# Kernel optimization log

Measured on AMD Instinct MI355X. Metric: run time of the kernel, lower is better.

Reference implementation:

```python
import jax, jax.numpy as jnp
import numpy as np

C = 512
H = 8

def setup_inputs() -> dict:
    key = jax.random.key(0)
    ks = jax.random.split(key, 5)
    x = jax.random.normal(ks[0], (4, C, 2048), dtype=jnp.float32)
    # Conv1d(kernel_size=1) == pointwise linear: weight [out, in], bias [out]
    qkv_w = jax.random.normal(ks[1], (3 * C, C), dtype=jnp.float32) * (1.0 / np.sqrt(C))
    qkv_b = jax.random.normal(ks[2], (3 * C,), dtype=jnp.float32) * 0.02
    proj_w = jax.random.normal(ks[3], (C, C), dtype=jnp.float32) * (1.0 / np.sqrt(C))
    proj_b = jax.random.normal(ks[4], (C,), dtype=jnp.float32) * 0.02
    return {"x": x, "qkv_w": qkv_w, "qkv_b": qkv_b, "proj_w": proj_w, "proj_b": proj_b}

def reference(x, qkv_w, qkv_b, proj_w, proj_b):
    b, c, t = x.shape
    scale = c ** (-0.5)  # NOTE: full channel count, matching the torch module
    # pointwise conv: [3C, C] @ [b, C, T] -> [b, 3C, T]
    qkv = jnp.einsum('oc,bct->bot', qkv_w, x) + qkv_b[None, :, None]
    q, k, v = jnp.split(qkv, 3, axis=1)
    d = c // H
    q = q.reshape(b, H, d, t)
    k = k.reshape(b, H, d, t)
    v = v.reshape(b, H, d, t)
    attn = jnp.einsum('bhct,bhcs->bhts', q, k) * scale
    attn = jax.nn.softmax(attn, axis=-1)
    out = jnp.einsum('bhts,bhcs->bhct', attn, v)
    out = out.reshape(b, c, t)
    out = jnp.einsum('oc,bct->bot', proj_w, out) + proj_b[None, :, None]
    return x + out
```

## Files before the change

### kernel.cpp

```cpp
#include <hip/hip_runtime.h>
#include <hip/hip_bf16.h>
#include <math.h>

#define B_DIM 4
#define C_DIM 512
#define T_DIM 2048
#define H_DIM 8
#define OC3   1536
#define VN_STRIDE 2064
#define SCALE 0.044194173824159216f
#define SCALE2 (0.044194173824159216f * 1.4426950408889634f)

typedef unsigned short ushortT;
typedef unsigned int uintT;
typedef __attribute__((ext_vector_type(8))) short bf16x8;
typedef __attribute__((ext_vector_type(4))) short bf16x4;
typedef __attribute__((ext_vector_type(4))) float f32x4;

__device__ __forceinline__ ushortT f2bf(float f) {
    union { float f; uintT u; } v; v.f = f;
    uintT r = v.u + 0x7FFF + ((v.u >> 16) & 1);
    return (ushortT)(r >> 16);
}
__device__ __forceinline__ float bf2f(ushortT h) {
    union { uintT u; float f; } v; v.u = ((uintT)h) << 16;
    return v.f;
}
__device__ __forceinline__ uintT pack2bf(float a, float b) {
    uintT ua = __float_as_uint(a) + 0x8000u;
    uintT ub = __float_as_uint(b) + 0x8000u;
    return (ua >> 16) | (ub & 0xFFFF0000u);
}
__device__ __forceinline__ uintT cvtpk2bf(float a, float b) {
    union { __bf16 v[2]; uintT u; } c;
    c.v[0] = (__bf16)a; c.v[1] = (__bf16)b;
    return c.u;
}
__device__ __forceinline__ void gload_lds16(const ushortT* g, ushortT* l) {
    __builtin_amdgcn_global_load_lds(
        (const __attribute__((address_space(1))) void*)g,
        (__attribute__((address_space(3))) void*)l, 16, 0, 0);
}

__global__ __launch_bounds__(256) void prep(const float* __restrict__ x,
                                            const float* __restrict__ qw,
                                            const float* __restrict__ pw,
                                            ushortT* __restrict__ xb,
                                            ushortT* __restrict__ qwb,
                                            ushortT* __restrict__ pwb) {
    __shared__ float xs[64][65];
    const int tid = threadIdx.x;
    const int blk = blockIdx.x;
    if (blk >= 1024) {
        int idx = ((blk - 1024) * 256 + tid) * 4;
        if (idx < OC3 * C_DIM) {
            float4 v = *(const float4*)(qw + idx);
            qwb[idx + 0] = f2bf(v.x); qwb[idx + 1] = f2bf(v.y);
            qwb[idx + 2] = f2bf(v.z); qwb[idx + 3] = f2bf(v.w);
        } else {
            idx -= OC3 * C_DIM;
            float4 v = *(const float4*)(pw + idx);
            pwb[idx + 0] = f2bf(v.x); pwb[idx + 1] = f2bf(v.y);
            pwb[idx + 2] = f2bf(v.z); pwb[idx + 3] = f2bf(v.w);
        }
        return;
    }
    const int b = blk >> 8, rem = blk & 255;
    const int c0 = (rem >> 5) * 64, t0 = (rem & 31) * 64;
    #pragma unroll
    for (int it = 0; it < 4; ++it) {
        int idx = it * 256 + tid;
        int r = idx >> 4, ch = idx & 15;
        float4 v = *(const float4*)(x + ((size_t)(b * C_DIM + c0 + r)) * T_DIM + t0 + ch * 4);
        xs[r][ch * 4 + 0] = v.x; xs[r][ch * 4 + 1] = v.y;
        xs[r][ch * 4 + 2] = v.z; xs[r][ch * 4 + 3] = v.w;
    }
    __syncthreads();
    #pragma unroll
    for (int it = 0; it < 2; ++it) {
        int idx = it * 256 + tid;
        int rt = idx >> 3, ch = idx & 7;
        union { ushortT s[8]; uint4 v; } tmp;
        #pragma unroll
        for (int k = 0; k < 8; ++k) tmp.s[k] = f2bf(xs[ch * 8 + k][rt]);
        *(uint4*)(xb + ((size_t)b * T_DIM + t0 + rt) * C_DIM + c0 + ch * 8) = tmp.v;
    }
}

__global__ __launch_bounds__(256, 3) void gemm_qkv(const ushortT* __restrict__ A,
                                                   const ushortT* __restrict__ Bw,
                                                   const float* __restrict__ bias,
                                                   ushortT* __restrict__ out,
                                                   ushortT* __restrict__ Vn) {
    __shared__ __align__(16) ushortT As[8192], Bs[8192];
    const int tid = threadIdx.x, lane = tid & 63, wid = tid >> 6;
    const int u = lane & 15, q = lane >> 4;
    const int wm = wid & 1, wn = wid >> 1;
    const int m0 = blockIdx.x * 128, n0 = blockIdx.y * 128;
    const int lrow = lane >> 2, lcol = (lane & 3) * 8;

    f32x4 acc[4][4];
    const f32x4 z = {0.f, 0.f, 0.f, 0.f};
    #pragma unroll
    for (int mi = 0; mi < 4; ++mi)
        #pragma unroll
        for (int ni = 0; ni < 4; ++ni) acc[mi][ni] = z;

    for (int k0 = 0; k0 < 512; k0 += 64) {
        __syncthreads();
        gload_lds16(A  + (size_t)(m0 + wid * 32 +      lrow) * 512 + k0      + lcol, &As[(wid * 32     ) * 32]);
        gload_lds16(A  + (size_t)(m0 + wid * 32 + 16 + lrow) * 512 + k0      + lcol, &As[(wid * 32 + 16) * 32]);
        gload_lds16(A  + (size_t)(m0 + wid * 32 +      lrow) * 512 + k0 + 32 + lcol, &As[4096 + (wid * 32     ) * 32]);
        gload_lds16(A  + (size_t)(m0 + wid * 32 + 16 + lrow) * 512 + k0 + 32 + lcol, &As[4096 + (wid * 32 + 16) * 32]);
        gload_lds16(Bw + (size_t)(n0 + wid * 32 +      lrow) * 512 + k0      + lcol, &Bs[(wid * 32     ) * 32]);
        gload_lds16(Bw + (size_t)(n0 + wid * 32 + 16 + lrow) * 512 + k0      + lcol, &Bs[(wid * 32 + 16) * 32]);
        gload_lds16(Bw + (size_t)(n0 + wid * 32 +      lrow) * 512 + k0 + 32 + lcol, &Bs[4096 + (wid * 32     ) * 32]);
        gload_lds16(Bw + (size_t)(n0 + wid * 32 + 16 + lrow) * 512 + k0 + 32 + lcol, &Bs[4096 + (wid * 32 + 16) * 32]);
        __syncthreads();
        bf16x8 af[4][2], bfr[4][2];
        #pragma unroll
        for (int mi = 0; mi < 4; ++mi) {
            af[mi][0] = *(const bf16x8*)&As[(wm * 64 + mi * 16 + u) * 32 + q * 8];
            af[mi][1] = *(const bf16x8*)&As[4096 + (wm * 64 + mi * 16 + u) * 32 + q * 8];
        }
        #pragma unroll
        for (int ni = 0; ni < 4; ++ni) {
            bfr[ni][0] = *(const bf16x8*)&Bs[(wn * 64 + ni * 16 + u) * 32 + q * 8];
            bfr[ni][1] = *(const bf16x8*)&Bs[4096 + (wn * 64 + ni * 16 + u) * 32 + q * 8];
        }
        #pragma unroll
        for (int mi = 0; mi < 4; ++mi)
            #pragma unroll
            for (int ni = 0; ni < 4; ++ni) {
                acc[mi][ni] = __builtin_amdgcn_mfma_f32_16x16x32_bf16(
                    af[mi][0], bfr[ni][0], acc[mi][ni], 0, 0, 0);
                acc[mi][ni] = __builtin_amdgcn_mfma_f32_16x16x32_bf16(
                    af[mi][1], bfr[ni][1], acc[mi][ni], 0, 0, 0);
            }
    }
    if (n0 < 1024) {
        const float scl = (n0 < 512) ? SCALE2 : 1.0f;
        #pragma unroll
        for (int ni = 0; ni < 4; ++ni) {
            int o = n0 + wn * 64 + ni * 16 + u;
            float bv = bias[o];
            #pragma unroll
            for (int mi = 0; mi < 4; ++mi)
                #pragma unroll
                for (int r = 0; r < 4; ++r) {
                    int m = m0 + wm * 64 + mi * 16 + q * 4 + r;
                    out[(size_t)m * OC3 + o] = f2bf((acc[mi][ni][r] + bv) * scl);
                }
        }
    } else {
        #pragma unroll
        for (int ni = 0; ni < 4; ++ni) {
            int o = n0 + wn * 64 + ni * 16 + u;
            float bv = bias[o];
            int oo = o - 1024;
            int hv = oo >> 6, d = oo & 63;
            #pragma unroll
            for (int mi = 0; mi < 4; ++mi) {
                int m = m0 + wm * 64 + mi * 16 + q * 4;
                int b = m >> 11, t = m & 2047;
                uint2 w;
                w.x = pack2bf(acc[mi][ni][0] + bv, acc[mi][ni][1] + bv);
                w.y = pack2bf(acc[mi][ni][2] + bv, acc[mi][ni][3] + bv);
                *(uint2*)(Vn + ((size_t)((b * 8 + hv) * 64 + d)) * VN_STRIDE + t) = w;
            }
        }
    }
}

__global__ __launch_bounds__(256, 2)
void flash(const ushortT* __restrict__ qkvT, const ushortT* __restrict__ Vn,
           ushortT* __restrict__ AO)
{
    __shared__ __align__(16) ushortT smem[16384];

    const int tid = threadIdx.x, lane = tid & 63, wid = tid >> 6;
    const int u = lane & 15, q = lane >> 4;
    const int g = blockIdx.x;
    const int bh = (g & 7) * 4 + ((g >> 3) & 3);
    const int qt = g >> 5;
    const int bb = bh >> 3, h = bh & 7;
    const int q0 = qt * 128;
    const size_t qbase = (size_t)bb * T_DIM * OC3;

    bf16x8 qb[2][2];
    #pragma unroll
    for (int ti = 0; ti < 2; ++ti)
        #pragma unroll
        for (int kst = 0; kst < 2; ++kst)
            qb[ti][kst] = *(const bf16x8*)(qkvT + qbase
                + (size_t)(q0 + wid * 32 + ti * 16 + u) * OC3 + h * 64 + kst * 32 + q * 8);

    const int rs = wid * 8 + (lane >> 3);
    const int sg = (lane & 7) ^ (rs & 7);
    const ushortT* ks0 = qkvT + qbase + (size_t)(rs     ) * OC3 + 512 + h * 64 + sg * 8;
    const ushortT* ks1 = qkvT + qbase + (size_t)(rs + 32) * OC3 + 512 + h * 64 + sg * 8;
    const ushortT* vs0 = Vn + ((size_t)bh * 64 + rs     ) * VN_STRIDE + sg * 8;
    const ushortT* vs1 = Vn + ((size_t)bh * 64 + rs + 32) * VN_STRIDE + sg * 8;

    f32x4 acc[4][2];
    const f32x4 z = {0.f, 0.f, 0.f, 0.f};
    #pragma unroll
    for (int ci = 0; ci < 4; ++ci)
        #pragma unroll
        for (int ti = 0; ti < 2; ++ti) acc[ci][ti] = z;
    f32x4 lacc[2] = {z, z};
    const bf16x4 ones = {(short)0x3F80, (short)0x3F80, (short)0x3F80, (short)0x3F80};

    gload_lds16(ks0, &smem[       wid * 512]);
    gload_lds16(ks1, &smem[2048 + wid * 512]);
    gload_lds16(vs0, &smem[8192 +        wid * 512]);
    gload_lds16(vs1, &smem[8192 + 2048 + wid * 512]);
    ks0 += 64 * OC3; ks1 += 64 * OC3; vs0 += 64; vs1 += 64;
    __syncthreads();

    int cur = 0;
    for (int rnd = 0; rnd < 32; ++rnd) {
        if (rnd < 31) {
            int nb = cur ^ 1;
            gload_lds16(ks0, &smem[nb * 4096 +        wid * 512]);
            gload_lds16(ks1, &smem[nb * 4096 + 2048 + wid * 512]);
            gload_lds16(vs0, &smem[8192 + nb * 4096 +        wid * 512]);
            gload_lds16(vs1, &smem[8192 + nb * 4096 + 2048 + wid * 512]);
            ks0 += 64 * OC3; ks1 += 64 * OC3; vs0 += 64; vs1 += 64;
        }
        const ushortT* Kb = &smem[cur * 4096];
        const ushortT* Vb = &smem[8192 + cur * 4096];
        bf16x8 ka[4][2];
        #pragma unroll
        for (int si = 0; si < 4; ++si)
            #pragma unroll
            for (int kst = 0; kst < 2; ++kst)
                ka[si][kst] = *(const bf16x8*)&Kb[(si * 16 + u) * 64
                    + (((kst * 4 + q) ^ (u & 7)) * 8)];
        bf16x4 va[4][4];
        #pragma unroll
        for (int si = 0; si < 4; ++si)
            #pragma unroll
            for (int ci = 0; ci < 4; ++ci)
                va[si][ci] = *(const bf16x4*)&Vb[(ci * 16 + u) * 64
                    + (((si * 2 + (q >> 1)) ^ (u & 7)) * 8) + (q & 1) * 4];

        #pragma unroll
        for (int si = 0; si < 4; ++si) {
            f32x4 sacc[2] = {z, z};
            #pragma unroll
            for (int ti = 0; ti < 2; ++ti)
                sacc[ti] = __builtin_amdgcn_mfma_f32_16x16x32_bf16(
                    ka[si][0], qb[ti][0], sacc[ti], 0, 0, 0);
            #pragma unroll
            for (int ti = 0; ti < 2; ++ti)
                sacc[ti] = __builtin_amdgcn_mfma_f32_16x16x32_bf16(
                    ka[si][1], qb[ti][1], sacc[ti], 0, 0, 0);
            #pragma unroll
            for (int ti = 0; ti < 2; ++ti) {
                float p0 = __builtin_amdgcn_exp2f(sacc[ti][0]);
                float p1 = __builtin_amdgcn_exp2f(sacc[ti][1]);
                float p2 = __builtin_amdgcn_exp2f(sacc[ti][2]);
                float p3 = __builtin_amdgcn_exp2f(sacc[ti][3]);
                union { uint2 u2; bf16x4 v; } pw;
                pw.u2.x = cvtpk2bf(p0, p1);
                pw.u2.y = cvtpk2bf(p2, p3);
                lacc[ti] = __builtin_amdgcn_mfma_f32_16x16x16bf16_1k(
                    ones, pw.v, lacc[ti], 0, 0, 0);
                #pragma unroll
                for (int ci = 0; ci < 4; ++ci)
                    acc[ci][ti] = __builtin_amdgcn_mfma_f32_16x16x16bf16_1k(
                        va[si][ci], pw.v, acc[ci][ti], 0, 0, 0);
            }
        }
        __syncthreads();
        cur ^= 1;
    }

    ushortT* Ob = smem + wid * 2304;
    float* Lb = (float*)(smem + 9216);
    if (q == 0) {
        Lb[wid * 32 + u]      = lacc[0][0];
        Lb[wid * 32 + 16 + u] = lacc[1][0];
    }
    #pragma unroll
    for (int ci = 0; ci < 4; ++ci)
        #pragma unroll
        for (int ti = 0; ti < 2; ++ti) {
            uint2 w;
            w.x = pack2bf(acc[ci][ti][0], acc[ci][ti][1]);
            w.y = pack2bf(acc[ci][ti][2], acc[ci][ti][3]);
            *(uint2*)&Ob[(ti * 16 + u) * 72 + ci * 16 + q * 4] = w;
        }
    __syncthreads();
    {
        const int row = tid >> 1, cs = (tid & 1) * 32;
        const int w = row >> 5, r32 = row & 31;
        float linv = 1.0f / Lb[w * 32 + r32];
        const ushortT* rp = smem + w * 2304 + r32 * 72 + cs;
        size_t orow = ((size_t)bb * T_DIM + q0 + row) * C_DIM + h * 64 + cs;
        #pragma unroll
        for (int j = 0; j < 4; ++j) {
            uint4 rv = *(const uint4*)(rp + j * 8);
            const uintT* rpp = (const uintT*)&rv;
            uint4 o;
            uintT* op = (uintT*)&o;
            #pragma unroll
            for (int k = 0; k < 4; ++k)
                op[k] = pack2bf(bf2f((ushortT)(rpp[k] & 0xFFFF)) * linv,
                                bf2f((ushortT)(rpp[k] >> 16)) * linv);
            *(uint4*)(AO + orow + j * 8) = o;
        }
    }
}

__global__ __launch_bounds__(256, 2) void gemm_proj(const ushortT* __restrict__ Wp,
                                                    const ushortT* __restrict__ AOv,
                                                    const float* __restrict__ bias,
                                                    const float* __restrict__ xres,
                                                    float* __restrict__ out) {
    __shared__ __align__(16) ushortT As[8192], Bs[4096];
    const int tid = threadIdx.x, lane = tid & 63, wid = tid >> 6;
    const int u = lane & 15, q = lane >> 4;
    const int wm = wid & 1, wn = wid >> 1;
    const int m0 = blockIdx.y * 128, n0 = blockIdx.x * 64;
    const int lrow = lane >> 2, lcol = (lane & 3) * 8;

    f32x4 acc[4][2];
    const f32x4 z = {0.f, 0.f, 0.f, 0.f};
    #pragma unroll
    for (int mi = 0; mi < 4; ++mi)
        #pragma unroll
        for (int ni = 0; ni < 2; ++ni) acc[mi][ni] = z;

    for (int k0 = 0; k0 < 512; k0 += 64) {
        __syncthreads();
        gload_lds16(Wp  + (size_t)(m0 + wid * 32 +      lrow) * 512 + k0      + lcol, &As[(wid * 32     ) * 32]);
        gload_lds16(Wp  + (size_t)(m0 + wid * 32 + 16 + lrow) * 512 + k0      + lcol, &As[(wid * 32 + 16) * 32]);
        gload_lds16(Wp  + (size_t)(m0 + wid * 32 +      lrow) * 512 + k0 + 32 + lcol, &As[4096 + (wid * 32     ) * 32]);
        gload_lds16(Wp  + (size_t)(m0 + wid * 32 + 16 + lrow) * 512 + k0 + 32 + lcol, &As[4096 + (wid * 32 + 16) * 32]);
        gload_lds16(AOv + (size_t)(n0 + wid * 16 + lrow) * 512 + k0      + lcol, &Bs[(wid * 16) * 32]);
        gload_lds16(AOv + (size_t)(n0 + wid * 16 + lrow) * 512 + k0 + 32 + lcol, &Bs[2048 + (wid * 16) * 32]);
        __syncthreads();
        bf16x8 af[4][2], bfr[2][2];
        #pragma unroll
        for (int mi = 0; mi < 4; ++mi) {
            af[mi][0] = *(const bf16x8*)&As[(wm * 64 + mi * 16 + u) * 32 + q * 8];
            af[mi][1] = *(const bf16x8*)&As[4096 + (wm * 64 + mi * 16 + u) * 32 + q * 8];
        }
        #pragma unroll
        for (int ni = 0; ni < 2; ++ni) {
            bfr[ni][0] = *(const bf16x8*)&Bs[(wn * 32 + ni * 16 + u) * 32 + q * 8];
            bfr[ni][1] = *(const bf16x8*)&Bs[2048 + (wn * 32 + ni * 16 + u) * 32 + q * 8];
        }
        #pragma unroll
        for (int mi = 0; mi < 4; ++mi)
            #pragma unroll
            for (int ni = 0; ni < 2; ++ni) {
                acc[mi][ni] = __builtin_amdgcn_mfma_f32_16x16x32_bf16(
                    af[mi][0], bfr[ni][0], acc[mi][ni], 0, 0, 0);
                acc[mi][ni] = __builtin_amdgcn_mfma_f32_16x16x32_bf16(
                    af[mi][1], bfr[ni][1], acc[mi][ni], 0, 0, 0);
            }
    }
    #pragma unroll
    for (int mi = 0; mi < 4; ++mi)
        #pragma unroll
        for (int r = 0; r < 4; ++r) {
            int o = m0 + wm * 64 + mi * 16 + q * 4 + r;
            float bv = bias[o];
            #pragma unroll
            for (int ni = 0; ni < 2; ++ni) {
                int n = n0 + wn * 32 + ni * 16 + u;
                int b = n >> 11, t = n & 2047;
                size_t oi = ((size_t)b * C_DIM + o) * T_DIM + t;
                out[oi] = acc[mi][ni][r] + bv + xres[oi];
            }
        }
}

extern "C" void kernel_launch(void* const* d_in, const int* in_sizes, int n_in,
                              void* d_out, int out_size, void* d_ws, size_t ws_size,
                              hipStream_t stream)
{
    const float* x      = (const float*)d_in[0];
    const float* qkv_w  = (const float*)d_in[1];
    const float* qkv_b  = (const float*)d_in[2];
    const float* proj_w = (const float*)d_in[3];
    const float* proj_b = (const float*)d_in[4];
    float* out = (float*)d_out;

    char* ws = (char*)d_ws;
    ushortT* xb   = (ushortT*)(ws);
    ushortT* wqb  = (ushortT*)(ws +  8388608);
    ushortT* wpb  = (ushortT*)(ws +  9961472);
    ushortT* qkvT = (ushortT*)(ws + 10485760);
    ushortT* Vn   = (ushortT*)(ws + 35651584);
    ushortT* AO   = (ushortT*)(ws + 44105728);

    prep     <<<2048, 256, 0, stream>>>(x, qkv_w, proj_w, xb, wqb, wpb);
    gemm_qkv <<<dim3(64, 12),   256, 0, stream>>>(xb, wqb, qkv_b, qkvT, Vn);
    flash    <<<512,            256, 0, stream>>>(qkvT, Vn, AO);
    gemm_proj<<<dim3(128, 4),   256, 0, stream>>>(wpb, AO, proj_b, x, out);
}
```

Baseline: 153.6 us.

## Triple-buffer K/V tiles in flash kernel with explicit vmcnt waits

Moves the flash attention K/V staging from double to triple buffering in LDS. Two tiles are prefetched ahead, and each iteration waits only for the oldest outstanding loads using s_waitcnt vmcnt(4) before a raw s_barrier, instead of a full __syncthreads. This is meant to hide global-to-LDS load latency behind the MFMA work. In exchange, LDS use grows from 32KB to 48KB per block, which may limit occupancy at two blocks per CU, and correctness now depends on the hand-written wait counts.

```diff
diff --git a/kernel.cpp b/kernel.cpp
--- a/kernel.cpp
+++ b/kernel.cpp
@@ -176,7 +176,7 @@
 void flash(const ushortT* __restrict__ qkvT, const ushortT* __restrict__ Vn,
            ushortT* __restrict__ AO)
 {
-    __shared__ __align__(16) ushortT smem[16384];
+    __shared__ __align__(16) ushortT smem[24576];
 
     const int tid = threadIdx.x, lane = tid & 63, wid = tid >> 6;
     const int u = lane & 15, q = lane >> 4;
@@ -202,6 +202,14 @@
     const ushortT* vs0 = Vn + ((size_t)bh * 64 + rs     ) * VN_STRIDE + sg * 8;
     const ushortT* vs1 = Vn + ((size_t)bh * 64 + rs + 32) * VN_STRIDE + sg * 8;
 
+    #define STAGE_F(kb) do { \
+        gload_lds16(ks0, &smem[(kb) * 4096 +        wid * 512]); \
+        gload_lds16(ks1, &smem[(kb) * 4096 + 2048 + wid * 512]); \
+        gload_lds16(vs0, &smem[12288 + (kb) * 4096 +        wid * 512]); \
+        gload_lds16(vs1, &smem[12288 + (kb) * 4096 + 2048 + wid * 512]); \
+        ks0 += 64 * OC3; ks1 += 64 * OC3; vs0 += 64; vs1 += 64; \
+    } while (0)
+
     f32x4 acc[4][2];
     const f32x4 z = {0.f, 0.f, 0.f, 0.f};
     #pragma unroll
@@ -211,25 +219,20 @@
     f32x4 lacc[2] = {z, z};
     const bf16x4 ones = {(short)0x3F80, (short)0x3F80, (short)0x3F80, (short)0x3F80};
 
-    gload_lds16(ks0, &smem[       wid * 512]);
-    gload_lds16(ks1, &smem[2048 + wid * 512]);
-    gload_lds16(vs0, &smem[8192 +        wid * 512]);
-    gload_lds16(vs1, &smem[8192 + 2048 + wid * 512]);
-    ks0 += 64 * OC3; ks1 += 64 * OC3; vs0 += 64; vs1 += 64;
-    __syncthreads();
-
-    int cur = 0;
-    for (int rnd = 0; rnd < 32; ++rnd) {
-        if (rnd < 31) {
-            int nb = cur ^ 1;
-            gload_lds16(ks0, &smem[nb * 4096 +        wid * 512]);
-            gload_lds16(ks1, &smem[nb * 4096 + 2048 + wid * 512]);
-            gload_lds16(vs0, &smem[8192 + nb * 4096 +        wid * 512]);
-            gload_lds16(vs1, &smem[8192 + nb * 4096 + 2048 + wid * 512]);
-            ks0 += 64 * OC3; ks1 += 64 * OC3; vs0 += 64; vs1 += 64;
-        }
-        const ushortT* Kb = &smem[cur * 4096];
-        const ushortT* Vb = &smem[8192 + cur * 4096];
+    STAGE_F(0);
+    STAGE_F(1);
+    asm volatile("s_waitcnt vmcnt(4)" ::: "memory");
+    __builtin_amdgcn_sched_barrier(0);
+    __builtin_amdgcn_s_barrier();
+
+    int b0 = 0;
+    for (int t = 0; t < 32; ++t) {
+        if (t < 30) {
+            int b2 = b0 + 2; if (b2 >= 3) b2 -= 3;
+            STAGE_F(b2);
+        }
+        const ushortT* Kb = &smem[b0 * 4096];
+        const ushortT* Vb = &smem[12288 + b0 * 4096];
         bf16x8 ka[4][2];
         #pragma unroll
         for (int si = 0; si < 4; ++si)
@@ -273,9 +276,13 @@
                         va[si][ci], pw.v, acc[ci][ti], 0, 0, 0);
             }
         }
-        __syncthreads();
-        cur ^= 1;
-    }
+        if (t < 30) asm volatile("s_waitcnt vmcnt(4)" ::: "memory");
+        else        asm volatile("s_waitcnt vmcnt(0)" ::: "memory");
+        __builtin_amdgcn_sched_barrier(0);
+        __builtin_amdgcn_s_barrier();
+        b0 += 1; if (b0 >= 3) b0 = 0;
+    }
+    #undef STAGE_F
 
     ushortT* Ob = smem + wid * 2304;
     float* Lb = (float*)(smem + 9216);
```

Result: no change. 154.9 us (+0.8%).
